# Performance work log

Measured on AMD Instinct MI355X. Metric: run time of the kernel, lower is better.

The kernel has to match this reference:

```python
import jax, jax.numpy as jnp
import numpy as np

T, B, F, H = 2048, 50, 750, 100  # time, batch(seen by LSTM), input feat, hidden
OUT = 2

def setup_inputs() -> dict:
    key = jax.random.key(0)
    ks = jax.random.split(key, 7)
    s = 1.0 / np.sqrt(H)
    u = lambda k, shape: jax.random.uniform(k, shape, jnp.float32, -s, s)
    return {
        "x": jax.random.normal(ks[0], (T, B, F), jnp.float32),
        "W_ih": u(ks[1], (4 * H, F)),
        "W_hh": u(ks[2], (4 * H, H)),
        "b_ih": u(ks[3], (4 * H,)),
        "b_hh": u(ks[4], (4 * H,)),
        "fc_W": u(ks[5], (OUT, B * H)),
        "fc_b": u(ks[6], (OUT,)),
    }

def reference(x, W_ih, W_hh, b_ih, b_hh, fc_W, fc_b):
    # PyTorch LSTM (batch_first=False): scan over dim0. Gate order: i, f, g, o.
    # Precompute input projections for all steps at once: (T, B, 4H)
    x_proj = jnp.einsum('tbf,gf->tbg', x, W_ih) + b_ih + b_hh

    def step(carry, xp):
        h, c = carry                      # (B, H) each
        gates = xp + h @ W_hh.T           # (B, 4H)
        i, f, g, o = jnp.split(gates, 4, axis=-1)
        i = jax.nn.sigmoid(i)
        f = jax.nn.sigmoid(f)
        g = jnp.tanh(g)
        o = jax.nn.sigmoid(o)
        c = f * c + i * g
        h = o * jnp.tanh(c)
        return (h, c), h

    h0 = jnp.zeros((B, H), x.dtype)
    c0 = jnp.zeros((B, H), x.dtype)
    _, hs = jax.lax.scan(step, (h0, c0), x_proj)  # hs: (T, B, H)
    flat = hs.reshape(hs.shape[0], -1)            # (T, B*H) == (T, 5000)
    return flat @ fc_W.T + fc_b                   # (T, 2)
```

## Files before the change

kernel.cpp:

```cpp
#include <hip/hip_runtime.h>

#define T_DIM 2048
#define B_DIM 50
#define F_DIM 750
#define H_DIM 100
#define G4    400
#define M_DIM (T_DIM * B_DIM)
#define KPAD  768

typedef __attribute__((ext_vector_type(8))) short short8v;
typedef __attribute__((ext_vector_type(4))) float f32x4;
typedef __attribute__((ext_vector_type(2))) float f32x2;

__device__ __forceinline__ float fast_rcp(float x) { return __builtin_amdgcn_rcpf(x); }
__device__ __forceinline__ float tanh_f(float x) {
    return 1.0f - 2.0f * fast_rcp(__expf(2.0f * x) + 1.0f);
}

__device__ __forceinline__ unsigned short f2bf_rne(float f) {
    unsigned int u = __float_as_uint(f);
    u = (u + 0x7FFFu + ((u >> 16) & 1u)) >> 16;
    return (unsigned short)u;
}
__device__ __forceinline__ float bf2f(unsigned short h) {
    return __uint_as_float(((unsigned int)h) << 16);
}

template <int CTRL>
__device__ __forceinline__ float qperm(float x) {
    return __int_as_float(__builtin_amdgcn_mov_dpp(__float_as_int(x), CTRL, 0xF, 0xF, false));
}

__global__ __launch_bounds__(256) void wconv(
    const float* __restrict__ W,
    unsigned short* __restrict__ Whi,
    unsigned short* __restrict__ Wlo)
{
    int i = blockIdx.x * 256 + threadIdx.x;
    if (i >= G4 * KPAD) return;
    int g = i / KPAD, k = i - g * KPAD;
    float v = (k < F_DIM) ? W[g * F_DIM + k] : 0.f;
    unsigned short h = f2bf_rne(v);
    Whi[i] = h;
    Wlo[i] = f2bf_rne(v - bf2f(h));
}

__global__ __launch_bounds__(512, 1) void xproj_mfma(
    const float* __restrict__ x,
    const unsigned short* __restrict__ Whi,
    const unsigned short* __restrict__ Wlo,
    const float* __restrict__ bih,
    const float* __restrict__ bhh,
    float* __restrict__ xp)
{
    const int m0   = blockIdx.x * 128;
    const int tid  = threadIdx.x;
    const int lane = tid & 63;
    const int w    = tid >> 6;
    const int rb   = (w >> 2) * 64;
    const int wc   = w & 3;
    const int fr   = lane & 15;
    const int fk   = (lane >> 4) * 8;

    __shared__ unsigned short Ahi[2][128][40];
    __shared__ unsigned short Alo[2][128][40];

    f32x4 acc[4][7];
    #pragma unroll
    for (int s = 0; s < 4; ++s)
        #pragma unroll
        for (int t = 0; t < 7; ++t)
            acc[s][t] = (f32x4){0.f, 0.f, 0.f, 0.f};

    float bias_t[7];
    #pragma unroll
    for (int tt = 0; tt < 7; ++tt) {
        const int nt = wc + 4 * tt;
        if (nt < 25) {
            const int n = nt * 16 + fr;
            bias_t[tt] = bih[n] + bhh[n];
        } else bias_t[tt] = 0.f;
    }

    const int sr = tid >> 2;
    const int sc = (tid & 3) * 8;
    const float* xrow = x + (size_t)(m0 + sr) * F_DIM;

    float f[8];

    #define STAGE_LOAD(KS)                                                     \
    {                                                                          \
        const int kg = (KS) * 32 + sc;                                         \
        _Pragma("unroll")                                                      \
        for (int i = 0; i < 8; i += 2) {                                       \
            if (kg + i + 1 < F_DIM) {                                          \
                float2 v = *reinterpret_cast<const float2*>(&xrow[kg + i]);    \
                f[i] = v.x; f[i + 1] = v.y;                                    \
            } else {                                                           \
                f[i]     = (kg + i < F_DIM) ? xrow[kg + i] : 0.f;              \
                f[i + 1] = 0.f;                                                \
            }                                                                  \
        }                                                                      \
    }

    #define STAGE_WRITE(NB)                                                    \
    {                                                                          \
        short8v vh, vl;                                                        \
        _Pragma("unroll")                                                      \
        for (int i = 0; i < 8; ++i) {                                          \
            unsigned int u = __float_as_uint(f[i]);                            \
            vh[i] = (short)(u >> 16);                                          \
            float r = f[i] - __uint_as_float(u & 0xffff0000u);                 \
            vl[i] = (short)(__float_as_uint(r) >> 16);                         \
        }                                                                      \
        *reinterpret_cast<short8v*>(&Ahi[NB][sr][sc]) = vh;                    \
        *reinterpret_cast<short8v*>(&Alo[NB][sr][sc]) = vl;                    \
    }

    STAGE_LOAD(0);
    STAGE_WRITE(0);
    asm volatile("s_waitcnt lgkmcnt(0)\ns_barrier" ::: "memory");

    for (int s = 0; s < 24; ++s) {
        const int cur = s & 1;
        short8v ah[4], al[4];
        #pragma unroll
        for (int st = 0; st < 4; ++st) {
            ah[st] = *reinterpret_cast<const short8v*>(&Ahi[cur][rb + st * 16 + fr][fk]);
            al[st] = *reinterpret_cast<const short8v*>(&Alo[cur][rb + st * 16 + fr][fk]);
        }

        if (s < 23) STAGE_LOAD(s + 1);

        const int kb = s * 32 + fk;
        #pragma unroll
        for (int tt = 0; tt < 7; ++tt) {
            const int nt = wc + 4 * tt;
            if (nt < 25) {
                const int n = nt * 16 + fr;
                const short8v bh = *reinterpret_cast<const short8v*>(&Whi[n * KPAD + kb]);
                const short8v bl = *reinterpret_cast<const short8v*>(&Wlo[n * KPAD + kb]);
                #pragma unroll
                for (int st = 0; st < 4; ++st) {
                    acc[st][tt] = __builtin_amdgcn_mfma_f32_16x16x32_bf16(ah[st], bh, acc[st][tt], 0, 0, 0);
                    acc[st][tt] = __builtin_amdgcn_mfma_f32_16x16x32_bf16(ah[st], bl, acc[st][tt], 0, 0, 0);
                    acc[st][tt] = __builtin_amdgcn_mfma_f32_16x16x32_bf16(al[st], bh, acc[st][tt], 0, 0, 0);
                }
            }
        }

        if (s < 23) STAGE_WRITE(cur ^ 1);
        asm volatile("s_waitcnt lgkmcnt(0)\ns_barrier" ::: "memory");
    }

    #pragma unroll
    for (int tt = 0; tt < 7; ++tt) {
        const int nt = wc + 4 * tt;
        if (nt < 25) {
            const int n = nt * 16 + fr;
            #pragma unroll
            for (int st = 0; st < 4; ++st) {
                #pragma unroll
                for (int r = 0; r < 4; ++r) {
                    const int m = m0 + rb + st * 16 + (lane >> 4) * 4 + r;
                    xp[(size_t)m * G4 + n] = acc[st][tt][r] + bias_t[tt];
                }
            }
        }
    }
    #undef STAGE_LOAD
    #undef STAGE_WRITE
}

__global__ __launch_bounds__(448, 1) void lstm_scan(
    const float* __restrict__ xp,
    const float* __restrict__ Whh,
    float* __restrict__ hs)
{
    const int b   = blockIdx.x;
    const int tid = threadIdx.x;
    const int q   = tid & 3;
    const int j   = tid >> 2;
    const int jc  = (j < H_DIM) ? j : (H_DIM - 1);
    const int row = q * H_DIM + jc;

    __shared__ __align__(16) float hbuf[2][112];

    f32x2 w2[4][14];
    #pragma unroll
    for (int g = 0; g < 4; ++g) {
        const float* base = Whh + (size_t)(g * H_DIM + jc) * H_DIM + 25 * q;
        #pragma unroll
        for (int r = 0; r < 12; ++r)
            w2[g][r] = (f32x2){base[2 * r], base[2 * r + 1]};
        w2[g][12] = (f32x2){base[24], 0.f};
        w2[g][13] = (f32x2){0.f, 0.f};
    }
    #pragma unroll
    for (int g = 0; g < 4; ++g)
        #pragma unroll
        for (int r = 0; r < 14; ++r)
            asm volatile("" : "+v"(w2[g][r]));

    if (tid < 112) { hbuf[0][tid] = 0.f; hbuf[1][tid] = 0.f; }

    const int hpos = (jc / 25) * 28 + (jc % 25);
    const bool writer = (q == 0) && (j < H_DIM);

    const float s_act = (q == 2) ? 2.0f : 1.0f;
    const float nsl2  = -s_act * 1.44269504088896f;
    const float nsm1  = 1.0f - s_act;

    float c = 0.f;
    const float* xp_ptr = xp + (size_t)b * G4 + row;
    float*       hs_ptr = hs + (size_t)b * H_DIM + j;
    const size_t xstride = (size_t)B_DIM * G4;

    float xpv   = xp_ptr[0];
    float xp_n1 = xp_ptr[xstride];
    __syncthreads();

    int p = 0;
    for (int t = 0; t < T_DIM; ++t) {
        float xp_n2 = 0.f;
        if (t + 2 < T_DIM) xp_n2 = xp_ptr[2 * xstride];
        xp_ptr += xstride;

        f32x2 a0 = {0.f, 0.f}, a1 = {0.f, 0.f}, a2 = {0.f, 0.f}, a3 = {0.f, 0.f};
        const float* hq = &hbuf[p][28 * q];
        #pragma unroll
        for (int k4 = 0; k4 < 7; ++k4) {
            float4 hv = *reinterpret_cast<const float4*>(hq + 4 * k4);
            f32x2 hlo = {hv.x, hv.y};
            f32x2 hhi = {hv.z, hv.w};
            a0 = __builtin_elementwise_fma(w2[0][2 * k4],     hlo, a0);
            a0 = __builtin_elementwise_fma(w2[0][2 * k4 + 1], hhi, a0);
            a1 = __builtin_elementwise_fma(w2[1][2 * k4],     hlo, a1);
            a1 = __builtin_elementwise_fma(w2[1][2 * k4 + 1], hhi, a1);
            a2 = __builtin_elementwise_fma(w2[2][2 * k4],     hlo, a2);
            a2 = __builtin_elementwise_fma(w2[2][2 * k4 + 1], hhi, a2);
            a3 = __builtin_elementwise_fma(w2[3][2 * k4],     hlo, a3);
            a3 = __builtin_elementwise_fma(w2[3][2 * k4 + 1], hhi, a3);
        }
        float ac0 = a0.x + a0.y + ((q == 0) ? xpv : 0.f);
        float ac1 = a1.x + a1.y + ((q == 1) ? xpv : 0.f);
        float ac2 = a2.x + a2.y + ((q == 2) ? xpv : 0.f);
        float ac3 = a3.x + a3.y + ((q == 3) ? xpv : 0.f);

        ac0 += qperm<0xB1>(ac0);
        ac1 += qperm<0xB1>(ac1);
        ac2 += qperm<0xB1>(ac2);
        ac3 += qperm<0xB1>(ac3);
        ac0 += qperm<0x4E>(ac0);
        ac1 += qperm<0x4E>(ac1);
        ac2 += qperm<0x4E>(ac2);
        ac3 += qperm<0x4E>(ac3);

        float pre = ac0;
        pre = (q == 1) ? ac1 : pre;
        pre = (q == 2) ? ac2 : pre;
        pre = (q == 3) ? ac3 : pre;
        float act = fmaf(s_act, fast_rcp(1.0f + __builtin_amdgcn_exp2f(nsl2 * pre)), nsm1);

        float i_ = qperm<0x00>(act);
        float f_ = qperm<0x55>(act);
        float g_ = qperm<0xAA>(act);
        float o_ = qperm<0xFF>(act);

        c = fmaf(f_, c, i_ * g_);
        const float h = o_ * tanh_f(c);

        if (writer) {
            hbuf[p ^ 1][hpos] = h;
            *hs_ptr = h;
        }
        hs_ptr += B_DIM * H_DIM;
        asm volatile("s_waitcnt lgkmcnt(0)\ns_barrier" ::: "memory");
        p ^= 1;
        xpv   = xp_n1;
        xp_n1 = xp_n2;
    }
}

__global__ __launch_bounds__(256) void fc_kernel(
    const float* __restrict__ hs,
    const float* __restrict__ fcW,
    const float* __restrict__ fcb,
    float* __restrict__ out)
{
    const int t   = blockIdx.x;
    const int tid = threadIdx.x;

    float p0 = 0.f, p1 = 0.f;
    for (int k = tid * 4; k < 5000; k += 1024) {
        const float4 hv = *reinterpret_cast<const float4*>(&hs[(size_t)t * 5000 + k]);
        const float4 w0 = *reinterpret_cast<const float4*>(&fcW[k]);
        const float4 w1 = *reinterpret_cast<const float4*>(&fcW[5000 + k]);
        p0 += hv.x * w0.x + hv.y * w0.y + hv.z * w0.z + hv.w * w0.w;
        p1 += hv.x * w1.x + hv.y * w1.y + hv.z * w1.z + hv.w * w1.w;
    }
    #pragma unroll
    for (int off = 32; off > 0; off >>= 1) {
        p0 += __shfl_xor(p0, off);
        p1 += __shfl_xor(p1, off);
    }
    __shared__ float red[8];
    const int wv = tid >> 6;
    if ((tid & 63) == 0) { red[wv * 2] = p0; red[wv * 2 + 1] = p1; }
    __syncthreads();
    if (tid == 0) {
        out[2 * t]     = fcb[0] + red[0] + red[2] + red[4] + red[6];
        out[2 * t + 1] = fcb[1] + red[1] + red[3] + red[5] + red[7];
    }
}

extern "C" void kernel_launch(void* const* d_in, const int* in_sizes, int n_in,
                              void* d_out, int out_size, void* d_ws, size_t ws_size,
                              hipStream_t stream) {
    const float* x   = (const float*)d_in[0];
    const float* Wih = (const float*)d_in[1];
    const float* Whh = (const float*)d_in[2];
    const float* bih = (const float*)d_in[3];
    const float* bhh = (const float*)d_in[4];
    const float* fcW = (const float*)d_in[5];
    const float* fcb = (const float*)d_in[6];
    float* out = (float*)d_out;

    char* ws = (char*)d_ws;
    float*          xp  = (float*)ws;
    unsigned short* Whi = (unsigned short*)(ws + (size_t)M_DIM * G4 * 4);
    unsigned short* Wlo = Whi + (size_t)G4 * KPAD;
    float*          hs  = (float*)((char*)(Wlo + (size_t)G4 * KPAD));

    wconv<<<(G4 * KPAD + 255) / 256, 256, 0, stream>>>(Wih, Whi, Wlo);

    xproj_mfma<<<M_DIM / 128, 512, 0, stream>>>(x, Whi, Wlo, bih, bhh, xp);

    lstm_scan<<<B_DIM, 448, 0, stream>>>(xp, Whh, hs);

    fc_kernel<<<T_DIM, 256, 0, stream>>>(hs, fcW, fcb, out);
}
```

Before: 1.664 ms.

## Give each scan thread one full gate row instead of a quarter-K slice

The LSTM scan is repartitioned so each thread owns one complete gate row of W_hh (100 weights in registers) and computes its full dot product against the whole h vector. This removes the cross-lane DPP reduction and the per-gate select chain that the old K-split layout needed. In exchange each thread does 50 packed FMAs per step on one serial chain pair, and every lane reads the full h from LDS as a broadcast. Scheduling barriers are also placed around the waitcnt+barrier asm to stop the compiler moving instructions across it.

```diff
diff --git a/kernel.cpp b/kernel.cpp
--- a/kernel.cpp
+++ b/kernel.cpp
@@ -29,6 +29,12 @@
 template <int CTRL>
 __device__ __forceinline__ float qperm(float x) {
     return __int_as_float(__builtin_amdgcn_mov_dpp(__float_as_int(x), CTRL, 0xF, 0xF, false));
+}
+
+__device__ __forceinline__ void lgkm_barrier() {
+    __builtin_amdgcn_sched_barrier(0);
+    asm volatile("s_waitcnt lgkmcnt(0)\ns_barrier" ::: "memory");
+    __builtin_amdgcn_sched_barrier(0);
 }
 
 __global__ __launch_bounds__(256) void wconv(
@@ -119,7 +125,7 @@
 
     STAGE_LOAD(0);
     STAGE_WRITE(0);
-    asm volatile("s_waitcnt lgkmcnt(0)\ns_barrier" ::: "memory");
+    lgkm_barrier();
 
     for (int s = 0; s < 24; ++s) {
         const int cur = s & 1;
@@ -150,7 +156,7 @@
         }
 
         if (s < 23) STAGE_WRITE(cur ^ 1);
-        asm volatile("s_waitcnt lgkmcnt(0)\ns_barrier" ::: "memory");
+        lgkm_barrier();
     }
 
     #pragma unroll
@@ -179,41 +185,35 @@
 {
     const int b   = blockIdx.x;
     const int tid = threadIdx.x;
-    const int q   = tid & 3;
+    const int g   = tid & 3;
     const int j   = tid >> 2;
     const int jc  = (j < H_DIM) ? j : (H_DIM - 1);
-    const int row = q * H_DIM + jc;
-
-    __shared__ __align__(16) float hbuf[2][112];
-
-    f32x2 w2[4][14];
-    #pragma unroll
-    for (int g = 0; g < 4; ++g) {
-        const float* base = Whh + (size_t)(g * H_DIM + jc) * H_DIM + 25 * q;
-        #pragma unroll
-        for (int r = 0; r < 12; ++r)
-            w2[g][r] = (f32x2){base[2 * r], base[2 * r + 1]};
-        w2[g][12] = (f32x2){base[24], 0.f};
-        w2[g][13] = (f32x2){0.f, 0.f};
-    }
-    #pragma unroll
-    for (int g = 0; g < 4; ++g)
-        #pragma unroll
-        for (int r = 0; r < 14; ++r)
-            asm volatile("" : "+v"(w2[g][r]));
-
-    if (tid < 112) { hbuf[0][tid] = 0.f; hbuf[1][tid] = 0.f; }
-
-    const int hpos = (jc / 25) * 28 + (jc % 25);
-    const bool writer = (q == 0) && (j < H_DIM);
-
-    const float s_act = (q == 2) ? 2.0f : 1.0f;
+    const int row = g * H_DIM + jc;
+
+    __shared__ __align__(16) float hbuf[2][H_DIM];
+
+    f32x2 w2[50];
+    {
+        const float* wrow = Whh + (size_t)row * H_DIM;
+        #pragma unroll
+        for (int i = 0; i < 25; ++i) {
+            float4 v = *reinterpret_cast<const float4*>(&wrow[4 * i]);
+            w2[2 * i]     = (f32x2){v.x, v.y};
+            w2[2 * i + 1] = (f32x2){v.z, v.w};
+        }
+    }
+
+    if (tid < H_DIM) { hbuf[0][tid] = 0.f; hbuf[1][tid] = 0.f; }
+
+    const bool writer = (g == 0) && (j < H_DIM);
+
+    const float s_act = (g == 2) ? 2.0f : 1.0f;
     const float nsl2  = -s_act * 1.44269504088896f;
     const float nsm1  = 1.0f - s_act;
 
     float c = 0.f;
     const float* xp_ptr = xp + (size_t)b * G4 + row;
-    float*       hs_ptr = hs + (size_t)b * H_DIM + j;
+    float*       hs_ptr = hs + (size_t)b * H_DIM + jc;
     const size_t xstride = (size_t)B_DIM * G4;
 
     float xpv   = xp_ptr[0];
@@ -226,56 +226,34 @@
         if (t + 2 < T_DIM) xp_n2 = xp_ptr[2 * xstride];
         xp_ptr += xstride;
 
-        f32x2 a0 = {0.f, 0.f}, a1 = {0.f, 0.f}, a2 = {0.f, 0.f}, a3 = {0.f, 0.f};
-        const float* hq = &hbuf[p][28 * q];
-        #pragma unroll
-        for (int k4 = 0; k4 < 7; ++k4) {
-            float4 hv = *reinterpret_cast<const float4*>(hq + 4 * k4);
-            f32x2 hlo = {hv.x, hv.y};
-            f32x2 hhi = {hv.z, hv.w};
-            a0 = __builtin_elementwise_fma(w2[0][2 * k4],     hlo, a0);
-            a0 = __builtin_elementwise_fma(w2[0][2 * k4 + 1], hhi, a0);
-            a1 = __builtin_elementwise_fma(w2[1][2 * k4],     hlo, a1);
-            a1 = __builtin_elementwise_fma(w2[1][2 * k4 + 1], hhi, a1);
-            a2 = __builtin_elementwise_fma(w2[2][2 * k4],     hlo, a2);
-            a2 = __builtin_elementwise_fma(w2[2][2 * k4 + 1], hhi, a2);
-            a3 = __builtin_elementwise_fma(w2[3][2 * k4],     hlo, a3);
-            a3 = __builtin_elementwise_fma(w2[3][2 * k4 + 1], hhi, a3);
-        }
-        float ac0 = a0.x + a0.y + ((q == 0) ? xpv : 0.f);
-        float ac1 = a1.x + a1.y + ((q == 1) ? xpv : 0.f);
-        float ac2 = a2.x + a2.y + ((q == 2) ? xpv : 0.f);
-        float ac3 = a3.x + a3.y + ((q == 3) ? xpv : 0.f);
-
-        ac0 += qperm<0xB1>(ac0);
-        ac1 += qperm<0xB1>(ac1);
-        ac2 += qperm<0xB1>(ac2);
-        ac3 += qperm<0xB1>(ac3);
-        ac0 += qperm<0x4E>(ac0);
-        ac1 += qperm<0x4E>(ac1);
-        ac2 += qperm<0x4E>(ac2);
-        ac3 += qperm<0x4E>(ac3);
-
-        float pre = ac0;
-        pre = (q == 1) ? ac1 : pre;
-        pre = (q == 2) ? ac2 : pre;
-        pre = (q == 3) ? ac3 : pre;
-        float act = fmaf(s_act, fast_rcp(1.0f + __builtin_amdgcn_exp2f(nsl2 * pre)), nsm1);
-
-        float i_ = qperm<0x00>(act);
-        float f_ = qperm<0x55>(act);
-        float g_ = qperm<0xAA>(act);
-        float o_ = qperm<0xFF>(act);
+        f32x2 a0 = {xpv, 0.f};
+        f32x2 a1 = {0.f, 0.f};
+        const float* hb = hbuf[p];
+        #pragma unroll
+        for (int k = 0; k < 25; ++k) {
+            float4 hv = *reinterpret_cast<const float4*>(&hb[4 * k]);
+            a0 = __builtin_elementwise_fma(w2[2 * k],     (f32x2){hv.x, hv.y}, a0);
+            a1 = __builtin_elementwise_fma(w2[2 * k + 1], (f32x2){hv.z, hv.w}, a1);
+        }
+        const float pre = (a0.x + a0.y) + (a1.x + a1.y);
+
+        const float act = fmaf(s_act,
+            fast_rcp(1.0f + __builtin_amdgcn_exp2f(nsl2 * pre)), nsm1);
+
+        const float i_ = qperm<0x00>(act);
+        const float f_ = qperm<0x55>(act);
+        const float g_ = qperm<0xAA>(act);
+        const float o_ = qperm<0xFF>(act);
 
         c = fmaf(f_, c, i_ * g_);
         const float h = o_ * tanh_f(c);
 
         if (writer) {
-            hbuf[p ^ 1][hpos] = h;
+            hbuf[p ^ 1][jc] = h;
             *hs_ptr = h;
         }
         hs_ptr += B_DIM * H_DIM;
-        asm volatile("s_waitcnt lgkmcnt(0)\ns_barrier" ::: "memory");
+        lgkm_barrier();
         p ^= 1;
         xpv   = xp_n1;
         xp_n1 = xp_n2;
```

Measured after the change: 1.646 ms. No clear change (-1.1%).
